# Kernel tuning notes

Measured on AMD Instinct MI355X. Metric: run time of the kernel, lower is better.

Reference implementation:

```python
import jax, jax.numpy as jnp
import numpy as np

N_IN = 64
N_HID = 128


def setup_inputs() -> dict:
    key = jax.random.key(0)
    k_x, k_wih, k_bih, k_whh, k_bhh = jax.random.split(key, 5)
    S, B = 1024, 4096
    x = jax.random.normal(k_x, (S, B, N_IN), dtype=jnp.float32)
    # torch.nn.Linear weights: W [out, in], b [out]
    lim_ih = 1.0 / np.sqrt(N_IN)
    lim_hh = 1.0 / np.sqrt(N_HID)
    W_ih = jax.random.uniform(k_wih, (N_HID, N_IN), jnp.float32, -lim_ih, lim_ih)
    b_ih = jax.random.uniform(k_bih, (N_HID,), jnp.float32, -lim_ih, lim_ih)
    W_hh = jax.random.uniform(k_whh, (N_HID, N_HID), jnp.float32, -lim_hh, lim_hh)
    b_hh = jax.random.uniform(k_bhh, (N_HID,), jnp.float32, -lim_hh, lim_hh)
    return {"x": x, "W_ih": W_ih, "b_ih": b_ih, "W_hh": W_hh, "b_hh": b_hh}


def reference(x, W_ih, b_ih, W_hh, b_hh):
    # Elman RNN: h_t = tanh(x_t @ W_ih^T + b_ih + h_{t-1} @ W_hh^T + b_hh)
    # x: [S, B, 64]; returns final hidden state [B, 128]
    B = x.shape[1]
    h0 = jnp.zeros((B, N_HID), dtype=x.dtype)
    # Precompute the input projection for all timesteps (one big GEMM).
    xp = jnp.einsum('sbi,hi->sbh', x, W_ih) + b_ih  # [S, B, 128]

    def step(h, xp_t):
        h_new = jnp.tanh(xp_t + h @ W_hh.T + b_hh)
        return h_new, None

    h_final, _ = jax.lax.scan(step, h0, xp)
    return h_final
```

## Files before the change

### kernel.cpp

```cpp
#include <hip/hip_runtime.h>

#define S_LEN 1024
#define BATCH 4096
#define NIN 64
#define NHID 128
#define BT 16

typedef __attribute__((ext_vector_type(8))) short bf16x8;
typedef __attribute__((ext_vector_type(4))) float f32x4;

__device__ __forceinline__ unsigned cvt_pk(float lo, float hi) {
    unsigned r;
    asm("v_cvt_pk_bf16_f32 %0, %1, %2" : "=v"(r) : "v"(lo), "v"(hi));
    return r;
}
__device__ __forceinline__ float tanh_fast(float z) {
    float u = __builtin_amdgcn_exp2f(z * 2.885390081777927f);
    return fmaf(-2.0f, __builtin_amdgcn_rcpf(u + 1.0f), 1.0f);
}
__device__ __forceinline__ void lds_barrier() {
    asm volatile("s_waitcnt lgkmcnt(0)\n\ts_barrier" ::: "memory");
}

#define MFMA __builtin_amdgcn_mfma_f32_16x16x32_bf16

__device__ __forceinline__ bf16x8 pack8(const f32x4& a, const f32x4& b) {
    union { bf16x8 v; unsigned u[4]; } r;
    r.u[0] = cvt_pk(a[0], a[1]); r.u[1] = cvt_pk(a[2], a[3]);
    r.u[2] = cvt_pk(b[0], b[1]); r.u[3] = cvt_pk(b[2], b[3]);
    return r.v;
}


__global__ __launch_bounds__(256, 1)
void rnn_kernel(const float* __restrict__ x,
                const float* __restrict__ W_ih,
                const float* __restrict__ b_ih,
                const float* __restrict__ W_hh,
                const float* __restrict__ b_hh,
                float* __restrict__ out)
{
    __shared__ __align__(16) char lds[8192];
    const int tid  = threadIdx.x;
    const int wv   = tid >> 6;
    const int lane = tid & 63;
    const int col  = lane & 15;
    const int kg   = lane >> 4;
    const int bb0  = blockIdx.x * BT;

    for (int i = tid; i < 2048; i += 256) ((int*)lds)[i] = 0;

    const int OWN = wv;
    char* lbx = lds + (lane << 4);
    char*       wp  = lbx + (OWN << 10);
    const char* rp1 = lbx + ((((OWN + 1) & 3)) << 10);
    const char* rp2 = lbx + ((((OWN + 2) & 3)) << 10);
    const char* rp3 = lbx + ((((OWN + 3) & 3)) << 10);

    bf16x8 whh0[4], whh1[4];
    const int tt0 = 2 * OWN, tt1 = tt0 + 1;
    #pragma unroll
    for (int q = 0; q < 4; ++q) {
        const int kkq = (OWN + q) & 3;
        {
            const float* pw = W_hh + (16 * tt0 + col) * NHID + 32 * kkq + 4 * kg;
            whh0[q] = pack8(*(const f32x4*)(pw), *(const f32x4*)(pw + 16));
        }
        {
            const float* pw = W_hh + (16 * tt1 + col) * NHID + 32 * kkq + 4 * kg;
            whh1[q] = pack8(*(const f32x4*)(pw), *(const f32x4*)(pw + 16));
        }
    }
    bf16x8 wihA0, wihB0, wihA1, wihB1;
    {
        const float* q0 = W_ih + (16 * tt0 + col) * NIN + 8 * kg;
        const float* q1 = W_ih + (16 * tt1 + col) * NIN + 8 * kg;
        wihA0 = pack8(*(const f32x4*)(q0),      *(const f32x4*)(q0 + 4));
        wihB0 = pack8(*(const f32x4*)(q0 + 32), *(const f32x4*)(q0 + 36));
        wihA1 = pack8(*(const f32x4*)(q1),      *(const f32x4*)(q1 + 4));
        wihB1 = pack8(*(const f32x4*)(q1 + 32), *(const f32x4*)(q1 + 36));
    }
    f32x4 bias0, bias1;
    {
        f32x4 bi = *(const f32x4*)(b_ih + 16 * tt0 + 4 * kg);
        f32x4 bh = *(const f32x4*)(b_hh + 16 * tt0 + 4 * kg);
        bias0 = bi + bh;
        bi = *(const f32x4*)(b_ih + 16 * tt1 + 4 * kg);
        bh = *(const f32x4*)(b_hh + 16 * tt1 + 4 * kg);
        bias1 = bi + bh;
    }

    const float* xlane = x + ((size_t)bb0 + col) * NIN + kg * 8;

    auto loadStage = [&](f32x4& v0, f32x4& v1, f32x4& v2, f32x4& v3, int t) {
        if (t < S_LEN) {
            const float* p = xlane + (size_t)t * (BATCH * NIN);
            v0 = *(const f32x4*)(p);      v1 = *(const f32x4*)(p + 4);
            v2 = *(const f32x4*)(p + 32); v3 = *(const f32x4*)(p + 36);
        }
    };
    auto computeXP = [&](const f32x4& v0, const f32x4& v1,
                         const f32x4& v2, const f32x4& v3,
                         f32x4& o0, f32x4& o1) {
        union { bf16x8 v; unsigned u[4]; } xa, xb;
        xa.u[0] = cvt_pk(v0[0], v0[1]); xa.u[1] = cvt_pk(v0[2], v0[3]);
        xa.u[2] = cvt_pk(v1[0], v1[1]); xa.u[3] = cvt_pk(v1[2], v1[3]);
        xb.u[0] = cvt_pk(v2[0], v2[1]); xb.u[1] = cvt_pk(v2[2], v2[3]);
        xb.u[2] = cvt_pk(v3[0], v3[1]); xb.u[3] = cvt_pk(v3[2], v3[3]);
        f32x4 p0 = bias0, p1 = bias1;
        p0 = MFMA(wihA0, xa.v, p0, 0, 0, 0);
        p1 = MFMA(wihA1, xa.v, p1, 0, 0, 0);
        p0 = MFMA(wihB0, xb.v, p0, 0, 0, 0);
        p1 = MFMA(wihB1, xb.v, p1, 0, 0, 0);
        o0 = p0; o1 = p1;
    };

    f32x4 S00, S01, S02, S03, S10, S11, S12, S13;
    f32x4 S20, S21, S22, S23, S30, S31, S32, S33;
    loadStage(S00, S01, S02, S03, 0);
    loadStage(S10, S11, S12, S13, 1);
    loadStage(S20, S21, S22, S23, 2);
    loadStage(S30, S31, S32, S33, 3);
    f32x4 xc0, xc1, xn0, xn1;
    computeXP(S00, S01, S02, S03, xc0, xc1);
    loadStage(S00, S01, S02, S03, 4);
    bf16x8 Bo = {0, 0, 0, 0, 0, 0, 0, 0};
    __syncthreads();

    auto cstep = [&](int t, f32x4& s0, f32x4& s1, f32x4& s2, f32x4& s3,
                     const f32x4& c0, const f32x4& c1,
                     f32x4& n0, f32x4& n1, bool last) {
        const int rb = (t & 1) << 12;
        bf16x8 P1 = *(const bf16x8*)(rp1 + rb);
        bf16x8 P2 = *(const bf16x8*)(rp2 + rb);
        bf16x8 P3 = *(const bf16x8*)(rp3 + rb);

        f32x4 a0 = c0, a1 = c1;
        a0 = MFMA(whh0[0], Bo, a0, 0, 0, 0);
        a1 = MFMA(whh1[0], Bo, a1, 0, 0, 0);

        computeXP(s0, s1, s2, s3, n0, n1);
        loadStage(s0, s1, s2, s3, t + 5);

        a0 = MFMA(whh0[1], P1, a0, 0, 0, 0);
        a1 = MFMA(whh1[1], P1, a1, 0, 0, 0);
        a0 = MFMA(whh0[2], P2, a0, 0, 0, 0);
        a1 = MFMA(whh1[2], P2, a1, 0, 0, 0);
        a0 = MFMA(whh0[3], P3, a0, 0, 0, 0);
        a1 = MFMA(whh1[3], P3, a1, 0, 0, 0);

        if (last) {
            #pragma unroll
            for (int i = 0; i < 4; ++i) a0[i] = tanh_fast(a0[i]);
            #pragma unroll
            for (int i = 0; i < 4; ++i) a1[i] = tanh_fast(a1[i]);
            float* ob = out + ((size_t)bb0 + col) * NHID + 32 * OWN + 4 * kg;
            *(f32x4*)(ob)      = a0;
            *(f32x4*)(ob + 16) = a1;
            lds_barrier();
            return;
        }
        #pragma unroll
        for (int i = 0; i < 4; ++i) a0[i] = tanh_fast(a0[i]);
        unsigned u0 = cvt_pk(a0[0], a0[1]);
        unsigned u1 = cvt_pk(a0[2], a0[3]);
        uint2 h0; h0.x = u0; h0.y = u1;
        char* wb = wp + (((t + 1) & 1) << 12);
        *(uint2*)(wb) = h0;
        #pragma unroll
        for (int i = 0; i < 4; ++i) a1[i] = tanh_fast(a1[i]);
        unsigned u2 = cvt_pk(a1[0], a1[1]);
        unsigned u3 = cvt_pk(a1[2], a1[3]);
        uint2 h1; h1.x = u2; h1.y = u3;
        *(uint2*)(wb + 8) = h1;
        union { bf16x8 v; unsigned u[4]; } fb;
        fb.u[0] = u0; fb.u[1] = u1; fb.u[2] = u2; fb.u[3] = u3;
        Bo = fb.v;
        lds_barrier();
    };

    for (int m = 0; m < 255; ++m) {
        const int t = 4 * m;
        cstep(t + 0, S10, S11, S12, S13, xc0, xc1, xn0, xn1, false);
        cstep(t + 1, S20, S21, S22, S23, xn0, xn1, xc0, xc1, false);
        cstep(t + 2, S30, S31, S32, S33, xc0, xc1, xn0, xn1, false);
        cstep(t + 3, S00, S01, S02, S03, xn0, xn1, xc0, xc1, false);
    }
    cstep(1020, S10, S11, S12, S13, xc0, xc1, xn0, xn1, false);
    cstep(1021, S20, S21, S22, S23, xn0, xn1, xc0, xc1, false);
    cstep(1022, S30, S31, S32, S33, xc0, xc1, xn0, xn1, false);
    cstep(1023, S00, S01, S02, S03, xn0, xn1, xc0, xc1, true);
}

extern "C" void kernel_launch(void* const* d_in, const int* in_sizes, int n_in,
                              void* d_out, int out_size, void* d_ws, size_t ws_size,
                              hipStream_t stream) {
    const float* x    = (const float*)d_in[0];
    const float* W_ih = (const float*)d_in[1];
    const float* b_ih = (const float*)d_in[2];
    const float* W_hh = (const float*)d_in[3];
    const float* b_hh = (const float*)d_in[4];
    float* out = (float*)d_out;

    dim3 grid(BATCH / BT);
    dim3 block(256);
    rnn_kernel<<<grid, block, 0, stream>>>(x, W_ih, b_ih, W_hh, b_hh, out);
}
```

Measured before the change: 480.2 us.

## Process two independent 16-row batch tiles per block to hide recurrence latency

Each block now handles 32 batch rows as two interleaved 16-row recurrences (A and B), doubling LDS and register state, and halving the grid to 128 blocks. Interleaving the independent MFMA chains is meant to hide the serial per-step MFMA/tanh/barrier latency by giving the scheduler two dependency chains per step. It also tweaks the tanh formula and adds a sched_barrier after each LDS barrier. The risks are higher register pressure and fewer blocks than CUs (128 blocks on a 256-CU part), which could leave half the device idle.

```diff
diff --git a/kernel.cpp b/kernel.cpp
--- a/kernel.cpp
+++ b/kernel.cpp
@@ -4,7 +4,7 @@
 #define BATCH 4096
 #define NIN 64
 #define NHID 128
-#define BT 16
+#define BT 32
 
 typedef __attribute__((ext_vector_type(8))) short bf16x8;
 typedef __attribute__((ext_vector_type(4))) float f32x4;
@@ -16,10 +16,11 @@
 }
 __device__ __forceinline__ float tanh_fast(float z) {
     float u = __builtin_amdgcn_exp2f(z * 2.885390081777927f);
-    return fmaf(-2.0f, __builtin_amdgcn_rcpf(u + 1.0f), 1.0f);
+    return (u - 1.0f) * __builtin_amdgcn_rcpf(u + 1.0f);
 }
 __device__ __forceinline__ void lds_barrier() {
     asm volatile("s_waitcnt lgkmcnt(0)\n\ts_barrier" ::: "memory");
+    __builtin_amdgcn_sched_barrier(0);
 }
 
 #define MFMA __builtin_amdgcn_mfma_f32_16x16x32_bf16
@@ -40,7 +41,7 @@
                 const float* __restrict__ b_hh,
                 float* __restrict__ out)
 {
-    __shared__ __align__(16) char lds[8192];
+    __shared__ __align__(16) char lds[16384];
     const int tid  = threadIdx.x;
     const int wv   = tid >> 6;
     const int lane = tid & 63;
@@ -48,14 +49,19 @@
     const int kg   = lane >> 4;
     const int bb0  = blockIdx.x * BT;
 
-    for (int i = tid; i < 2048; i += 256) ((int*)lds)[i] = 0;
+    for (int i = tid; i < 4096; i += 256) ((int*)lds)[i] = 0;
 
     const int OWN = wv;
-    char* lbx = lds + (lane << 4);
-    char*       wp  = lbx + (OWN << 10);
-    const char* rp1 = lbx + ((((OWN + 1) & 3)) << 10);
-    const char* rp2 = lbx + ((((OWN + 2) & 3)) << 10);
-    const char* rp3 = lbx + ((((OWN + 3) & 3)) << 10);
+    char* lbxA = lds + (lane << 4);
+    char* lbxB = lbxA + 8192;
+    char*       wpA  = lbxA + (OWN << 10);
+    const char* rpA1 = lbxA + ((((OWN + 1) & 3)) << 10);
+    const char* rpA2 = lbxA + ((((OWN + 2) & 3)) << 10);
+    const char* rpA3 = lbxA + ((((OWN + 3) & 3)) << 10);
+    char*       wpB  = lbxB + (OWN << 10);
+    const char* rpB1 = lbxB + ((((OWN + 1) & 3)) << 10);
+    const char* rpB2 = lbxB + ((((OWN + 2) & 3)) << 10);
+    const char* rpB3 = lbxB + ((((OWN + 3) & 3)) << 10);
 
     bf16x8 whh0[4], whh1[4];
     const int tt0 = 2 * OWN, tt1 = tt0 + 1;
@@ -90,11 +96,13 @@
         bias1 = bi + bh;
     }
 
-    const float* xlane = x + ((size_t)bb0 + col) * NIN + kg * 8;
-
-    auto loadStage = [&](f32x4& v0, f32x4& v1, f32x4& v2, f32x4& v3, int t) {
+    const float* xlaneA = x + ((size_t)bb0 + col) * NIN + kg * 8;
+    const float* xlaneB = x + ((size_t)bb0 + 16 + col) * NIN + kg * 8;
+
+    auto loadStage = [&](const float* xl,
+                         f32x4& v0, f32x4& v1, f32x4& v2, f32x4& v3, int t) {
         if (t < S_LEN) {
-            const float* p = xlane + (size_t)t * (BATCH * NIN);
+            const float* p = xl + (size_t)t * (BATCH * NIN);
             v0 = *(const f32x4*)(p);      v1 = *(const f32x4*)(p + 4);
             v2 = *(const f32x4*)(p + 32); v3 = *(const f32x4*)(p + 36);
         }
@@ -115,81 +123,120 @@
         o0 = p0; o1 = p1;
     };
 
-    f32x4 S00, S01, S02, S03, S10, S11, S12, S13;
-    f32x4 S20, S21, S22, S23, S30, S31, S32, S33;
-    loadStage(S00, S01, S02, S03, 0);
-    loadStage(S10, S11, S12, S13, 1);
-    loadStage(S20, S21, S22, S23, 2);
-    loadStage(S30, S31, S32, S33, 3);
-    f32x4 xc0, xc1, xn0, xn1;
-    computeXP(S00, S01, S02, S03, xc0, xc1);
-    loadStage(S00, S01, S02, S03, 4);
-    bf16x8 Bo = {0, 0, 0, 0, 0, 0, 0, 0};
+    f32x4 SA00, SA01, SA02, SA03, SA10, SA11, SA12, SA13;
+    f32x4 SA20, SA21, SA22, SA23, SA30, SA31, SA32, SA33;
+    f32x4 SB00, SB01, SB02, SB03, SB10, SB11, SB12, SB13;
+    f32x4 SB20, SB21, SB22, SB23, SB30, SB31, SB32, SB33;
+    loadStage(xlaneA, SA00, SA01, SA02, SA03, 0);
+    loadStage(xlaneA, SA10, SA11, SA12, SA13, 1);
+    loadStage(xlaneA, SA20, SA21, SA22, SA23, 2);
+    loadStage(xlaneA, SA30, SA31, SA32, SA33, 3);
+    loadStage(xlaneB, SB00, SB01, SB02, SB03, 0);
+    loadStage(xlaneB, SB10, SB11, SB12, SB13, 1);
+    loadStage(xlaneB, SB20, SB21, SB22, SB23, 2);
+    loadStage(xlaneB, SB30, SB31, SB32, SB33, 3);
+    f32x4 xcA0, xcA1, xnA0, xnA1, xcB0, xcB1, xnB0, xnB1;
+    computeXP(SA00, SA01, SA02, SA03, xcA0, xcA1);
+    loadStage(xlaneA, SA00, SA01, SA02, SA03, 4);
+    computeXP(SB00, SB01, SB02, SB03, xcB0, xcB1);
+    loadStage(xlaneB, SB00, SB01, SB02, SB03, 4);
+    bf16x8 BoA = {0, 0, 0, 0, 0, 0, 0, 0};
+    bf16x8 BoB = {0, 0, 0, 0, 0, 0, 0, 0};
     __syncthreads();
 
-    auto cstep = [&](int t, f32x4& s0, f32x4& s1, f32x4& s2, f32x4& s3,
-                     const f32x4& c0, const f32x4& c1,
-                     f32x4& n0, f32x4& n1, bool last) {
+    auto cstep = [&](int t,
+                     f32x4& sa0, f32x4& sa1, f32x4& sa2, f32x4& sa3,
+                     f32x4& sb0, f32x4& sb1, f32x4& sb2, f32x4& sb3,
+                     const f32x4& cA0, const f32x4& cA1, f32x4& nA0, f32x4& nA1,
+                     const f32x4& cB0, const f32x4& cB1, f32x4& nB0, f32x4& nB1,
+                     bool last) {
         const int rb = (t & 1) << 12;
-        bf16x8 P1 = *(const bf16x8*)(rp1 + rb);
-        bf16x8 P2 = *(const bf16x8*)(rp2 + rb);
-        bf16x8 P3 = *(const bf16x8*)(rp3 + rb);
-
-        f32x4 a0 = c0, a1 = c1;
-        a0 = MFMA(whh0[0], Bo, a0, 0, 0, 0);
-        a1 = MFMA(whh1[0], Bo, a1, 0, 0, 0);
-
-        computeXP(s0, s1, s2, s3, n0, n1);
-        loadStage(s0, s1, s2, s3, t + 5);
-
-        a0 = MFMA(whh0[1], P1, a0, 0, 0, 0);
-        a1 = MFMA(whh1[1], P1, a1, 0, 0, 0);
-        a0 = MFMA(whh0[2], P2, a0, 0, 0, 0);
-        a1 = MFMA(whh1[2], P2, a1, 0, 0, 0);
-        a0 = MFMA(whh0[3], P3, a0, 0, 0, 0);
-        a1 = MFMA(whh1[3], P3, a1, 0, 0, 0);
+        bf16x8 PA1 = *(const bf16x8*)(rpA1 + rb);
+        bf16x8 PA2 = *(const bf16x8*)(rpA2 + rb);
+        bf16x8 PA3 = *(const bf16x8*)(rpA3 + rb);
+        bf16x8 PB1 = *(const bf16x8*)(rpB1 + rb);
+        bf16x8 PB2 = *(const bf16x8*)(rpB2 + rb);
+        bf16x8 PB3 = *(const bf16x8*)(rpB3 + rb);
+
+        f32x4 aA0 = cA0, aA1 = cA1, aB0 = cB0, aB1 = cB1;
+        aA0 = MFMA(whh0[0], BoA, aA0, 0, 0, 0);
+        aA1 = MFMA(whh1[0], BoA, aA1, 0, 0, 0);
+        aB0 = MFMA(whh0[0], BoB, aB0, 0, 0, 0);
+        aB1 = MFMA(whh1[0], BoB, aB1, 0, 0, 0);
+
+        computeXP(sa0, sa1, sa2, sa3, nA0, nA1);
+        loadStage(xlaneA, sa0, sa1, sa2, sa3, t + 5);
+        computeXP(sb0, sb1, sb2, sb3, nB0, nB1);
+        loadStage(xlaneB, sb0, sb1, sb2, sb3, t + 5);
+
+        aA0 = MFMA(whh0[1], PA1, aA0, 0, 0, 0);
+        aB0 = MFMA(whh0[1], PB1, aB0, 0, 0, 0);
+        aA1 = MFMA(whh1[1], PA1, aA1, 0, 0, 0);
+        aB1 = MFMA(whh1[1], PB1, aB1, 0, 0, 0);
+        aA0 = MFMA(whh0[2], PA2, aA0, 0, 0, 0);
+        aB0 = MFMA(whh0[2], PB2, aB0, 0, 0, 0);
+        aA1 = MFMA(whh1[2], PA2, aA1, 0, 0, 0);
+        aB1 = MFMA(whh1[2], PB2, aB1, 0, 0, 0);
+        aA0 = MFMA(whh0[3], PA3, aA0, 0, 0, 0);
+        aB0 = MFMA(whh0[3], PB3, aB0, 0, 0, 0);
+        aA1 = MFMA(whh1[3], PA3, aA1, 0, 0, 0);
+        aB1 = MFMA(whh1[3], PB3, aB1, 0, 0, 0);
+
+        #pragma unroll
+        for (int i = 0; i < 4; ++i) aA0[i] = tanh_fast(aA0[i]);
+        #pragma unroll
+        for (int i = 0; i < 4; ++i) aB0[i] = tanh_fast(aB0[i]);
+        #pragma unroll
+        for (int i = 0; i < 4; ++i) aA1[i] = tanh_fast(aA1[i]);
+        #pragma unroll
+        for (int i = 0; i < 4; ++i) aB1[i] = tanh_fast(aB1[i]);
 
         if (last) {
-            #pragma unroll
-            for (int i = 0; i < 4; ++i) a0[i] = tanh_fast(a0[i]);
-            #pragma unroll
-            for (int i = 0; i < 4; ++i) a1[i] = tanh_fast(a1[i]);
-            float* ob = out + ((size_t)bb0 + col) * NHID + 32 * OWN + 4 * kg;
-            *(f32x4*)(ob)      = a0;
-            *(f32x4*)(ob + 16) = a1;
+            float* obA = out + ((size_t)bb0 + col) * NHID + 32 * OWN + 4 * kg;
+            float* obB = out + ((size_t)bb0 + 16 + col) * NHID + 32 * OWN + 4 * kg;
+            *(f32x4*)(obA)      = aA0;
+            *(f32x4*)(obA + 16) = aA1;
+            *(f32x4*)(obB)      = aB0;
+            *(f32x4*)(obB + 16) = aB1;
             lds_barrier();
             return;
         }
-        #pragma unroll
-        for (int i = 0; i < 4; ++i) a0[i] = tanh_fast(a0[i]);
-        unsigned u0 = cvt_pk(a0[0], a0[1]);
-        unsigned u1 = cvt_pk(a0[2], a0[3]);
-        uint2 h0; h0.x = u0; h0.y = u1;
-        char* wb = wp + (((t + 1) & 1) << 12);
-        *(uint2*)(wb) = h0;
-        #pragma unroll
-        for (int i = 0; i < 4; ++i) a1[i] = tanh_fast(a1[i]);
-        unsigned u2 = cvt_pk(a1[0], a1[1]);
-        unsigned u3 = cvt_pk(a1[2], a1[3]);
-        uint2 h1; h1.x = u2; h1.y = u3;
-        *(uint2*)(wb + 8) = h1;
-        union { bf16x8 v; unsigned u[4]; } fb;
-        fb.u[0] = u0; fb.u[1] = u1; fb.u[2] = u2; fb.u[3] = u3;
-        Bo = fb.v;
+        {
+            union { bf16x8 v; unsigned u[4]; } fb;
+            fb.u[0] = cvt_pk(aA0[0], aA0[1]); fb.u[1] = cvt_pk(aA0[2], aA0[3]);
+            fb.u[2] = cvt_pk(aA1[0], aA1[1]); fb.u[3] = cvt_pk(aA1[2], aA1[3]);
+            BoA = fb.v;
+            *(bf16x8*)(wpA + (((t + 1) & 1) << 12)) = BoA;
+        }
+        {
+            union { bf16x8 v; unsigned u[4]; } fb;
+            fb.u[0] = cvt_pk(aB0[0], aB0[1]); fb.u[1] = cvt_pk(aB0[2], aB0[3]);
+            fb.u[2] = cvt_pk(aB1[0], aB1[1]); fb.u[3] = cvt_pk(aB1[2], aB1[3]);
+            BoB = fb.v;
+            *(bf16x8*)(wpB + (((t + 1) & 1) << 12)) = BoB;
+        }
         lds_barrier();
     };
 
     for (int m = 0; m < 255; ++m) {
         const int t = 4 * m;
-        cstep(t + 0, S10, S11, S12, S13, xc0, xc1, xn0, xn1, false);
-        cstep(t + 1, S20, S21, S22, S23, xn0, xn1, xc0, xc1, false);
-        cstep(t + 2, S30, S31, S32, S33, xc0, xc1, xn0, xn1, false);
-        cstep(t + 3, S00, S01, S02, S03, xn0, xn1, xc0, xc1, false);
-    }
-    cstep(1020, S10, S11, S12, S13, xc0, xc1, xn0, xn1, false);
-    cstep(1021, S20, S21, S22, S23, xn0, xn1, xc0, xc1, false);
-    cstep(1022, S30, S31, S32, S33, xc0, xc1, xn0, xn1, false);
-    cstep(1023, S00, S01, S02, S03, xn0, xn1, xc0, xc1, true);
+        cstep(t + 0, SA10, SA11, SA12, SA13, SB10, SB11, SB12, SB13,
+              xcA0, xcA1, xnA0, xnA1, xcB0, xcB1, xnB0, xnB1, false);
+        cstep(t + 1, SA20, SA21, SA22, SA23, SB20, SB21, SB22, SB23,
+              xnA0, xnA1, xcA0, xcA1, xnB0, xnB1, xcB0, xcB1, false);
+        cstep(t + 2, SA30, SA31, SA32, SA33, SB30, SB31, SB32, SB33,
+              xcA0, xcA1, xnA0, xnA1, xcB0, xcB1, xnB0, xnB1, false);
+        cstep(t + 3, SA00, SA01, SA02, SA03, SB00, SB01, SB02, SB03,
+              xnA0, xnA1, xcA0, xcA1, xnB0, xnB1, xcB0, xcB1, false);
+    }
+    cstep(1020, SA10, SA11, SA12, SA13, SB10, SB11, SB12, SB13,
+          xcA0, xcA1, xnA0, xnA1, xcB0, xcB1, xnB0, xnB1, false);
+    cstep(1021, SA20, SA21, SA22, SA23, SB20, SB21, SB22, SB23,
+          xnA0, xnA1, xcA0, xcA1, xnB0, xnB1, xcB0, xcB1, false);
+    cstep(1022, SA30, SA31, SA32, SA33, SB30, SB31, SB32, SB33,
+          xcA0, xcA1, xnA0, xnA1, xcB0, xcB1, xnB0, xnB1, false);
+    cstep(1023, SA00, SA01, SA02, SA03, SB00, SB01, SB02, SB03,
+          xnA0, xnA1, xcA0, xcA1, xnB0, xnB1, xcB0, xcB1, true);
 }
 
 extern "C" void kernel_launch(void* const* d_in, const int* in_sizes, int n_in,
```

Result: slower. 898.1 us (+87.0%).
